# Kernel tuning notes

Hardware: AMD Instinct MI355X
Metric: run time of the kernel (lower is better)

Reference implementation:

```python
import jax, jax.numpy as jnp
import numpy as np

COLUMNS = 1024
CELLS = 16
NUM_CELLS = COLUMNS * CELLS
SEGS = 32
SYNS = 128
PERM_THR = 0.5
ACT_THR = 10
VOL_LR = 0.1


def _predictive(conn, vol, cons, active):
    # conn: [N,S,Y] int, vol/cons: [N,S,Y] float, active: [N] bool -> [N] bool
    connected = (vol > PERM_THR) | (cons > PERM_THR)
    pre = active[jnp.clip(conn, 0, NUM_CELLS - 1)]
    cnt = jnp.sum(connected & pre, axis=-1)          # active synapses per segment
    return jnp.any(cnt >= ACT_THR, axis=-1)         # cell predictive if any segment fires


def setup_inputs() -> dict:
    key = jax.random.key(0)
    k1, k2, k3, k4, k5 = jax.random.split(key, 5)
    x = jax.random.randint(k1, (COLUMNS,), 0, 2, dtype=jnp.int32)
    prev_active_cells = jax.random.bernoulli(k2, 0.5, (NUM_CELLS,))
    distal_connections = jax.random.randint(k3, (NUM_CELLS, SEGS, SYNS), 0, NUM_CELLS, dtype=jnp.int32)
    volatile_permanences = jax.random.uniform(k4, (NUM_CELLS, SEGS, SYNS), dtype=jnp.float32)
    consolidated_permanences = jax.random.uniform(k5, (NUM_CELLS, SEGS, SYNS), dtype=jnp.float32)
    return {
        'x': x,
        'modulation_signal': jnp.float32(1.0),
        'prev_active_cells': prev_active_cells,
        'distal_connections': distal_connections,
        'volatile_permanences': volatile_permanences,
        'consolidated_permanences': consolidated_permanences,
    }


def reference(x, modulation_signal, prev_active_cells, distal_connections,
              volatile_permanences, consolidated_permanences):
    col_active = x > 0                                              # [C]
    pred1 = _predictive(distal_connections, volatile_permanences,
                        consolidated_permanences, prev_active_cells).reshape(COLUMNS, CELLS)
    col_has_pred = jnp.any(pred1, axis=-1)                          # [C]
    cell_mask = jnp.where(col_has_pred[:, None], pred1, True)       # burst if no prediction
    new_active = (cell_mask & col_active[:, None]).reshape(-1)      # [N] bool (= winner cells)
    n_act = jnp.sum(col_active)
    n_pred = jnp.sum(col_active & col_has_pred)
    acc = jnp.where(n_act > 0,
                    n_pred.astype(jnp.float32) / jnp.maximum(n_act, 1).astype(jnp.float32),
                    jnp.float32(1.0))
    # Phase 2: learn on best-matching segment of each winner cell (volatile permanences)
    pre_prev = prev_active_cells[jnp.clip(distal_connections, 0, NUM_CELLS - 1)]  # [N,S,Y]
    overlaps = jnp.sum(pre_prev, axis=-1)                           # [N,S]
    best_seg = jnp.argmax(overlaps, axis=-1)                        # [N]
    seg_sel = best_seg[:, None] == jnp.arange(SEGS)[None, :]        # [N,S] bool
    learn_on = (modulation_signal != 0.0) & jnp.any(prev_active_cells)
    upd = new_active[:, None, None] & seg_sel[:, :, None] & learn_on  # [N,S,Y]
    delta = modulation_signal * VOL_LR * jnp.where(pre_prev, 1.0, -1.0)
    vol2 = jnp.clip(volatile_permanences + jnp.where(upd, delta, 0.0), 0.0, 1.0)
    # Phase 3: predictive state for next step, computed from new active cells
    pred2 = _predictive(distal_connections, vol2,
                        consolidated_permanences, new_active).reshape(COLUMNS, CELLS)
    new_predictive = (pred2 & col_active[:, None]).reshape(-1)
    return new_active, new_predictive, acc
```

## Files before the change

kernel.cpp:

```cpp
#include <hip/hip_runtime.h>
#include <stdint.h>

#define COLUMNS   1024
#define CELLS     16
#define NUM_CELLS (COLUMNS * CELLS)
#define SEGS      32
#define SYNS      128
#define ACT_THR   10
#define NB        2048
#define NWAVES    (NB * 4)

typedef int            i32x4 __attribute__((ext_vector_type(4)));
typedef float          f32x4 __attribute__((ext_vector_type(4)));

template<typename T>
__device__ __forceinline__ T ntload(const T* p) { return __builtin_nontemporal_load(p); }

__global__ __launch_bounds__(256) void pack_kernel(
    const void* __restrict__ prev, uint32_t* __restrict__ prevbits)
{
    __shared__ int s_isu8;
    const int t = threadIdx.x;
    if (t == 0) s_isu8 = 0;
    __syncthreads();
    const int* pi = (const int*)prev;
    int bad = 0;
    for (int k = t; k < NUM_CELLS / 4; k += 256)
        bad |= ((unsigned)pi[k] > 1u) ? 1 : 0;
    unsigned long long bb = __ballot(bad != 0);
    if ((t & 63) == 0 && bb) atomicOr(&s_isu8, 1);
    __syncthreads();

    if (t < 32) {
        const int w = blockIdx.x * 32 + t;
        uint32_t m = 0;
        if (s_isu8) {
            const unsigned char* p = (const unsigned char*)prev + (size_t)w * 32;
            #pragma unroll
            for (int j = 0; j < 32; ++j) m |= (p[j] ? 1u : 0u) << j;
        } else {
            const int* p = pi + (size_t)w * 32;
            #pragma unroll
            for (int j = 0; j < 32; ++j) m |= (p[j] ? 1u : 0u) << j;
        }
        prevbits[w] = m;
    }
}

__global__ __launch_bounds__(256) void p1_kernel(
    const uint32_t* __restrict__ prevbits, const int* __restrict__ x,
    const int* __restrict__ conn, const float* __restrict__ vol,
    const float* __restrict__ cons,
    unsigned char* __restrict__ pred1, unsigned char* __restrict__ bestseg)
{
    __shared__ uint32_t sbits[NUM_CELLS / 32];
    __shared__ unsigned short sacols[COLUMNS];
    __shared__ int s_gcnt[16], s_goff[16], s_acount;
    const int t = threadIdx.x, wv = t >> 6, ln = t & 63;

    for (int i = t; i < NUM_CELLS / 32; i += 256) sbits[i] = prevbits[i];

    int ca_[4];
    #pragma unroll
    for (int c2 = 0; c2 < 4; ++c2) {
        const int col = c2 * 256 + t;
        ca_[c2] = (x[col] != 0) ? 1 : 0;
        unsigned long long b = __ballot(ca_[c2] != 0);
        if (ln == 0) s_gcnt[c2 * 4 + wv] = __popcll(b);
    }
    __syncthreads();
    if (t == 0) {
        int s = 0;
        #pragma unroll
        for (int g = 0; g < 16; ++g) { s_goff[g] = s; s += s_gcnt[g]; }
        s_acount = s;
    }
    __syncthreads();
    #pragma unroll
    for (int c2 = 0; c2 < 4; ++c2) {
        unsigned long long b = __ballot(ca_[c2] != 0);
        if (ca_[c2])
            sacols[s_goff[c2 * 4 + wv] + __popcll(b & ((1ULL << ln) - 1ULL))] =
                (unsigned short)(c2 * 256 + t);
    }
    __syncthreads();

    const int nc   = s_acount * CELLS;
    const int half = ln >> 5;
    const int l32  = ln & 31;
    const int gw   = blockIdx.x * 4 + wv;

    for (int idx = gw; idx < nc; idx += NWAVES) {
        const int cell = (int)sacols[idx >> 4] * CELLS + (idx & 15);
        const size_t base = (size_t)cell * (SEGS * SYNS);
        int fire = 0, bestkey = 0;
        #pragma unroll 4
        for (int k = 0; k < 16; ++k) {
            const int segA = k * 2;
            const size_t off = base + (size_t)(segA + half) * SYNS + l32 * 4;
            i32x4 c = ntload((const i32x4*)(conn + off));
            int i0 = min(max(c.x, 0), NUM_CELLS - 1);
            int i1 = min(max(c.y, 0), NUM_CELLS - 1);
            int i2 = min(max(c.z, 0), NUM_CELLS - 1);
            int i3 = min(max(c.w, 0), NUM_CELLS - 1);
            int p0 = (sbits[i0 >> 5] >> (i0 & 31)) & 1;
            int p1 = (sbits[i1 >> 5] >> (i1 & 31)) & 1;
            int p2 = (sbits[i2 >> 5] >> (i2 & 31)) & 1;
            int p3 = (sbits[i3 >> 5] >> (i3 & 31)) & 1;
            unsigned long long bp0 = __ballot(p0 != 0);
            unsigned long long bp1 = __ballot(p1 != 0);
            unsigned long long bp2 = __ballot(p2 != 0);
            unsigned long long bp3 = __ballot(p3 != 0);
            int oA = __popcll(bp0 & 0xFFFFFFFFull) + __popcll(bp1 & 0xFFFFFFFFull)
                   + __popcll(bp2 & 0xFFFFFFFFull) + __popcll(bp3 & 0xFFFFFFFFull);
            int oB = __popcll(bp0 >> 32) + __popcll(bp1 >> 32)
                   + __popcll(bp2 >> 32) + __popcll(bp3 >> 32);
            bestkey = max(bestkey, (oA << 8) | (255 - segA));
            bestkey = max(bestkey, (oB << 8) | (254 - segA));
            if (!fire) {
                f32x4 v = ntload((const f32x4*)(vol + off));
                f32x4 q = ntload((const f32x4*)(cons + off));
                int cn0 = ((v.x > 0.5f) || (q.x > 0.5f)) ? 1 : 0;
                int cn1 = ((v.y > 0.5f) || (q.y > 0.5f)) ? 1 : 0;
                int cn2 = ((v.z > 0.5f) || (q.z > 0.5f)) ? 1 : 0;
                int cn3 = ((v.w > 0.5f) || (q.w > 0.5f)) ? 1 : 0;
                unsigned long long bc0 = __ballot(cn0 && p0);
                unsigned long long bc1 = __ballot(cn1 && p1);
                unsigned long long bc2 = __ballot(cn2 && p2);
                unsigned long long bc3 = __ballot(cn3 && p3);
                int cA = __popcll(bc0 & 0xFFFFFFFFull) + __popcll(bc1 & 0xFFFFFFFFull)
                       + __popcll(bc2 & 0xFFFFFFFFull) + __popcll(bc3 & 0xFFFFFFFFull);
                int cB = __popcll(bc0 >> 32) + __popcll(bc1 >> 32)
                       + __popcll(bc2 >> 32) + __popcll(bc3 >> 32);
                fire |= (cA >= ACT_THR) | (cB >= ACT_THR);
            }
        }
        if (ln == 0) {
            pred1[cell]   = (unsigned char)(fire ? 1 : 0);
            bestseg[cell] = (unsigned char)(255 - (bestkey & 0xFF));
        }
    }
}

__global__ __launch_bounds__(256) void p3_kernel(
    const uint32_t* __restrict__ prevbits, const int* __restrict__ x,
    const float* __restrict__ mod, const int* __restrict__ conn,
    const float* __restrict__ vol, const float* __restrict__ cons,
    const unsigned char* __restrict__ pred1, const unsigned char* __restrict__ bestseg,
    float* __restrict__ out)
{
    __shared__ uint32_t sprev[NUM_CELLS / 32];
    __shared__ uint32_t snew[NUM_CELLS / 32];
    __shared__ unsigned short sacols[COLUMNS];
    __shared__ unsigned short s_na[COLUMNS];
    __shared__ unsigned char s_act[COLUMNS];
    __shared__ int s_any, s_gcnt[16], s_goff[16], s_acount, s_nact, s_npred;
    const int t = threadIdx.x, wv = t >> 6, ln = t & 63;
    if (t == 0) { s_any = 0; s_nact = 0; s_npred = 0; }
    __syncthreads();

    {
        int any = 0;
        for (int i = t; i < NUM_CELLS / 32; i += 256) {
            uint32_t m = prevbits[i];
            sprev[i] = m;
            any |= (m != 0) ? 1 : 0;
        }
        unsigned long long ba = __ballot(any != 0);
        if (ln == 0 && ba) atomicOr(&s_any, 1);
    }

    int ca_[4];
    #pragma unroll
    for (int c2 = 0; c2 < 4; ++c2) {
        const int col = c2 * 256 + t;
        const int ca = (x[col] != 0) ? 1 : 0;
        ca_[c2] = ca;
        s_act[col] = (unsigned char)ca;
        uint4 pv = *(const uint4*)(pred1 + (size_t)col * CELLS);
        const int hp = ((pv.x | pv.y | pv.z | pv.w) != 0) ? 1 : 0;
        unsigned int bits = 0;
        if (ca) {
            if (hp) {
                #pragma unroll
                for (int b = 0; b < 4; ++b) {
                    unsigned int w = (&pv.x)[b];
                    bits |= ((w & 0xFFu) ? 1u : 0u) << (b * 4 + 0);
                    bits |= ((w & 0xFF00u) ? 1u : 0u) << (b * 4 + 1);
                    bits |= ((w & 0xFF0000u) ? 1u : 0u) << (b * 4 + 2);
                    bits |= ((w & 0xFF000000u) ? 1u : 0u) << (b * 4 + 3);
                }
            } else bits = 0xFFFFu;
        }
        s_na[col] = (unsigned short)bits;
        unsigned long long b1 = __ballot(ca != 0);
        unsigned long long b2 = __ballot((ca && hp) != 0);
        if (ln == 0) {
            s_gcnt[c2 * 4 + wv] = __popcll(b1);
            if (blockIdx.x == 0) {
                atomicAdd(&s_nact, __popcll(b1));
                atomicAdd(&s_npred, __popcll(b2));
            }
        }
    }
    __syncthreads();
    for (int w = t; w < NUM_CELLS / 32; w += 256)
        snew[w] = (uint32_t)s_na[2 * w] | ((uint32_t)s_na[2 * w + 1] << 16);
    if (t == 0) {
        int s = 0;
        #pragma unroll
        for (int g = 0; g < 16; ++g) { s_goff[g] = s; s += s_gcnt[g]; }
        s_acount = s;
    }
    __syncthreads();
    #pragma unroll
    for (int c2 = 0; c2 < 4; ++c2) {
        unsigned long long b = __ballot(ca_[c2] != 0);
        if (ca_[c2])
            sacols[s_goff[c2 * 4 + wv] + __popcll(b & ((1ULL << ln) - 1ULL))] =
                (unsigned short)(c2 * 256 + t);
    }

    float* outpred = out + NUM_CELLS;
    {
        const int i = blockIdx.x * 256 + t;
        if (i < NUM_CELLS && !s_act[i >> 4]) outpred[i] = 0.0f;
    }
    if (blockIdx.x == 0) {
        for (int g = t; g < NUM_CELLS / 4; g += 256) {
            const uint32_t w = snew[g >> 3];
            const int sh = (g & 7) * 4;
            f32x4 o;
            o.x = (w >> (sh + 0)) & 1 ? 1.0f : 0.0f;
            o.y = (w >> (sh + 1)) & 1 ? 1.0f : 0.0f;
            o.z = (w >> (sh + 2)) & 1 ? 1.0f : 0.0f;
            o.w = (w >> (sh + 3)) & 1 ? 1.0f : 0.0f;
            *(f32x4*)(out + (size_t)g * 4) = o;
        }
    }
    __syncthreads();
    if (blockIdx.x == 0 && t == 0)
        out[2 * NUM_CELLS] = (s_nact > 0)
            ? (float)s_npred / (float)max(s_nact, 1) : 1.0f;

    const int nc   = s_acount * CELLS;
    const int lf   = ((mod[0] != 0.0f) && s_any) ? 1 : 0;
    const float d  = mod[0] * 0.1f;
    const int half = ln >> 5;
    const int l32  = ln & 31;
    const int gw   = blockIdx.x * 4 + wv;

    for (int idx = gw; idx < nc; idx += NWAVES) {
        const int cell = (int)sacols[idx >> 4] * CELLS + (idx & 15);
        const size_t base = (size_t)cell * (SEGS * SYNS);
        const int na  = (snew[cell >> 5] >> (cell & 31)) & 1;
        const int upd = (lf && na) ? (int)bestseg[cell] : -1;
        int fire = 0;
        for (int k = 0; k < 16; ++k) {
            const int seg = k * 2 + half;
            const size_t off = base + (size_t)seg * SYNS + l32 * 4;
            i32x4 c = ntload((const i32x4*)(conn + off));
            f32x4 v = ntload((const f32x4*)(vol + off));
            f32x4 q = ntload((const f32x4*)(cons + off));
            int i0 = min(max(c.x, 0), NUM_CELLS - 1);
            int i1 = min(max(c.y, 0), NUM_CELLS - 1);
            int i2 = min(max(c.z, 0), NUM_CELLS - 1);
            int i3 = min(max(c.w, 0), NUM_CELLS - 1);
            float vx = v.x, vy = v.y, vz = v.z, vw = v.w;
            if (seg == upd) {
                int pp0 = (sprev[i0 >> 5] >> (i0 & 31)) & 1;
                int pp1 = (sprev[i1 >> 5] >> (i1 & 31)) & 1;
                int pp2 = (sprev[i2 >> 5] >> (i2 & 31)) & 1;
                int pp3 = (sprev[i3 >> 5] >> (i3 & 31)) & 1;
                vx += pp0 ? d : -d; vy += pp1 ? d : -d;
                vz += pp2 ? d : -d; vw += pp3 ? d : -d;
            }
            int cn0 = (vx > 0.5f) || (q.x > 0.5f);
            int cn1 = (vy > 0.5f) || (q.y > 0.5f);
            int cn2 = (vz > 0.5f) || (q.z > 0.5f);
            int cn3 = (vw > 0.5f) || (q.w > 0.5f);
            int pn0 = (snew[i0 >> 5] >> (i0 & 31)) & 1;
            int pn1 = (snew[i1 >> 5] >> (i1 & 31)) & 1;
            int pn2 = (snew[i2 >> 5] >> (i2 & 31)) & 1;
            int pn3 = (snew[i3 >> 5] >> (i3 & 31)) & 1;
            unsigned long long b0 = __ballot(cn0 && pn0);
            unsigned long long b1 = __ballot(cn1 && pn1);
            unsigned long long b2 = __ballot(cn2 && pn2);
            unsigned long long b3 = __ballot(cn3 && pn3);
            int cA = __popcll(b0 & 0xFFFFFFFFull) + __popcll(b1 & 0xFFFFFFFFull)
                   + __popcll(b2 & 0xFFFFFFFFull) + __popcll(b3 & 0xFFFFFFFFull);
            int cB = __popcll(b0 >> 32) + __popcll(b1 >> 32)
                   + __popcll(b2 >> 32) + __popcll(b3 >> 32);
            fire |= (cA >= ACT_THR) | (cB >= ACT_THR);
            if (fire) break;
        }
        if (ln == 0) outpred[cell] = fire ? 1.0f : 0.0f;
    }
}

extern "C" void kernel_launch(void* const* d_in, const int* in_sizes, int n_in,
                              void* d_out, int out_size, void* d_ws, size_t ws_size,
                              hipStream_t stream) {
    const int*   x    = (const int*)d_in[0];
    const float* mod  = (const float*)d_in[1];
    const void*  prev = d_in[2];
    const int*   conn = (const int*)d_in[3];
    const float* vol  = (const float*)d_in[4];
    const float* cons = (const float*)d_in[5];
    float* out = (float*)d_out;

    char* ws = (char*)d_ws;
    uint32_t* prevbits       = (uint32_t*)(ws + 0);
    unsigned char* pred1     = (unsigned char*)(ws + 16384);
    unsigned char* bestseg   = (unsigned char*)(ws + 32768);

    pack_kernel<<<16, 256, 0, stream>>>(prev, prevbits);
    p1_kernel<<<NB, 256, 0, stream>>>(prevbits, x, conn, vol, cons, pred1, bestseg);
    p3_kernel<<<NB, 256, 0, stream>>>(prevbits, x, mod, conn, vol, cons, pred1,
                                      bestseg, out);
}
```

Before: 51.60 us.

## Peel first segment in p1, skip vol/cons loads once fired, pack predictions as bits

The p1 kernel now evaluates segment pair 0 up front, including the connected check. If that pair already fires, the remaining segments only load connections for the best-segment overlap and skip the volatile and consolidated permanence reads. Phase-1 predictions become a bitmask built with atomicOr and cleared in pack_kernel, which makes the per-column check in p3 simpler. Nontemporal loads are replaced with ordinary loads in both kernels, which changes caching between p1 and p3, and the atomics add some contention.

```diff
diff --git a/kernel.cpp b/kernel.cpp
--- a/kernel.cpp
+++ b/kernel.cpp
@@ -13,11 +13,9 @@
 typedef int            i32x4 __attribute__((ext_vector_type(4)));
 typedef float          f32x4 __attribute__((ext_vector_type(4)));
 
-template<typename T>
-__device__ __forceinline__ T ntload(const T* p) { return __builtin_nontemporal_load(p); }
-
 __global__ __launch_bounds__(256) void pack_kernel(
-    const void* __restrict__ prev, uint32_t* __restrict__ prevbits)
+    const void* __restrict__ prev, uint32_t* __restrict__ prevbits,
+    uint32_t* __restrict__ predw)
 {
     __shared__ int s_isu8;
     const int t = threadIdx.x;
@@ -44,6 +42,7 @@
             for (int j = 0; j < 32; ++j) m |= (p[j] ? 1u : 0u) << j;
         }
         prevbits[w] = m;
+        predw[w] = 0;
     }
 }
 
@@ -51,7 +50,7 @@
     const uint32_t* __restrict__ prevbits, const int* __restrict__ x,
     const int* __restrict__ conn, const float* __restrict__ vol,
     const float* __restrict__ cons,
-    unsigned char* __restrict__ pred1, unsigned char* __restrict__ bestseg)
+    uint32_t* __restrict__ predw, unsigned char* __restrict__ bestseg)
 {
     __shared__ uint32_t sbits[NUM_CELLS / 32];
     __shared__ unsigned short sacols[COLUMNS];
@@ -94,11 +93,12 @@
         const int cell = (int)sacols[idx >> 4] * CELLS + (idx & 15);
         const size_t base = (size_t)cell * (SEGS * SYNS);
         int fire = 0, bestkey = 0;
-        #pragma unroll 4
-        for (int k = 0; k < 16; ++k) {
-            const int segA = k * 2;
-            const size_t off = base + (size_t)(segA + half) * SYNS + l32 * 4;
-            i32x4 c = ntload((const i32x4*)(conn + off));
+
+        {
+            const size_t off = base + (size_t)half * SYNS + l32 * 4;
+            i32x4 c = *(const i32x4*)(conn + off);
+            f32x4 v = *(const f32x4*)(vol + off);
+            f32x4 q = *(const f32x4*)(cons + off);
             int i0 = min(max(c.x, 0), NUM_CELLS - 1);
             int i1 = min(max(c.y, 0), NUM_CELLS - 1);
             int i2 = min(max(c.z, 0), NUM_CELLS - 1);
@@ -107,46 +107,111 @@
             int p1 = (sbits[i1 >> 5] >> (i1 & 31)) & 1;
             int p2 = (sbits[i2 >> 5] >> (i2 & 31)) & 1;
             int p3 = (sbits[i3 >> 5] >> (i3 & 31)) & 1;
+            int cn0 = ((v.x > 0.5f) || (q.x > 0.5f)) ? 1 : 0;
+            int cn1 = ((v.y > 0.5f) || (q.y > 0.5f)) ? 1 : 0;
+            int cn2 = ((v.z > 0.5f) || (q.z > 0.5f)) ? 1 : 0;
+            int cn3 = ((v.w > 0.5f) || (q.w > 0.5f)) ? 1 : 0;
+            unsigned long long bc0 = __ballot(cn0 && p0);
+            unsigned long long bc1 = __ballot(cn1 && p1);
+            unsigned long long bc2 = __ballot(cn2 && p2);
+            unsigned long long bc3 = __ballot(cn3 && p3);
             unsigned long long bp0 = __ballot(p0 != 0);
             unsigned long long bp1 = __ballot(p1 != 0);
             unsigned long long bp2 = __ballot(p2 != 0);
             unsigned long long bp3 = __ballot(p3 != 0);
+            int cA = __popcll(bc0 & 0xFFFFFFFFull) + __popcll(bc1 & 0xFFFFFFFFull)
+                   + __popcll(bc2 & 0xFFFFFFFFull) + __popcll(bc3 & 0xFFFFFFFFull);
+            int cB = __popcll(bc0 >> 32) + __popcll(bc1 >> 32)
+                   + __popcll(bc2 >> 32) + __popcll(bc3 >> 32);
             int oA = __popcll(bp0 & 0xFFFFFFFFull) + __popcll(bp1 & 0xFFFFFFFFull)
                    + __popcll(bp2 & 0xFFFFFFFFull) + __popcll(bp3 & 0xFFFFFFFFull);
             int oB = __popcll(bp0 >> 32) + __popcll(bp1 >> 32)
                    + __popcll(bp2 >> 32) + __popcll(bp3 >> 32);
-            bestkey = max(bestkey, (oA << 8) | (255 - segA));
-            bestkey = max(bestkey, (oB << 8) | (254 - segA));
-            if (!fire) {
-                f32x4 v = ntload((const f32x4*)(vol + off));
-                f32x4 q = ntload((const f32x4*)(cons + off));
-                int cn0 = ((v.x > 0.5f) || (q.x > 0.5f)) ? 1 : 0;
-                int cn1 = ((v.y > 0.5f) || (q.y > 0.5f)) ? 1 : 0;
-                int cn2 = ((v.z > 0.5f) || (q.z > 0.5f)) ? 1 : 0;
-                int cn3 = ((v.w > 0.5f) || (q.w > 0.5f)) ? 1 : 0;
-                unsigned long long bc0 = __ballot(cn0 && p0);
-                unsigned long long bc1 = __ballot(cn1 && p1);
-                unsigned long long bc2 = __ballot(cn2 && p2);
-                unsigned long long bc3 = __ballot(cn3 && p3);
-                int cA = __popcll(bc0 & 0xFFFFFFFFull) + __popcll(bc1 & 0xFFFFFFFFull)
-                       + __popcll(bc2 & 0xFFFFFFFFull) + __popcll(bc3 & 0xFFFFFFFFull);
-                int cB = __popcll(bc0 >> 32) + __popcll(bc1 >> 32)
-                       + __popcll(bc2 >> 32) + __popcll(bc3 >> 32);
-                fire |= (cA >= ACT_THR) | (cB >= ACT_THR);
+            fire = (cA >= ACT_THR) | (cB >= ACT_THR);
+            bestkey = max((oA << 8) | 255, (oB << 8) | 254);
+        }
+
+        if (fire) {
+            #pragma unroll
+            for (int k = 1; k < 16; ++k) {
+                const int segA = k * 2;
+                const size_t off = base + (size_t)(segA + half) * SYNS + l32 * 4;
+                i32x4 c = *(const i32x4*)(conn + off);
+                int i0 = min(max(c.x, 0), NUM_CELLS - 1);
+                int i1 = min(max(c.y, 0), NUM_CELLS - 1);
+                int i2 = min(max(c.z, 0), NUM_CELLS - 1);
+                int i3 = min(max(c.w, 0), NUM_CELLS - 1);
+                int p0 = (sbits[i0 >> 5] >> (i0 & 31)) & 1;
+                int p1 = (sbits[i1 >> 5] >> (i1 & 31)) & 1;
+                int p2 = (sbits[i2 >> 5] >> (i2 & 31)) & 1;
+                int p3 = (sbits[i3 >> 5] >> (i3 & 31)) & 1;
+                unsigned long long bp0 = __ballot(p0 != 0);
+                unsigned long long bp1 = __ballot(p1 != 0);
+                unsigned long long bp2 = __ballot(p2 != 0);
+                unsigned long long bp3 = __ballot(p3 != 0);
+                int oA = __popcll(bp0 & 0xFFFFFFFFull) + __popcll(bp1 & 0xFFFFFFFFull)
+                       + __popcll(bp2 & 0xFFFFFFFFull) + __popcll(bp3 & 0xFFFFFFFFull);
+                int oB = __popcll(bp0 >> 32) + __popcll(bp1 >> 32)
+                       + __popcll(bp2 >> 32) + __popcll(bp3 >> 32);
+                bestkey = max(bestkey, (oA << 8) | (255 - segA));
+                bestkey = max(bestkey, (oB << 8) | (254 - segA));
             }
-        }
+        } else {
+            #pragma unroll 4
+            for (int k = 1; k < 16; ++k) {
+                const int segA = k * 2;
+                const size_t off = base + (size_t)(segA + half) * SYNS + l32 * 4;
+                i32x4 c = *(const i32x4*)(conn + off);
+                int i0 = min(max(c.x, 0), NUM_CELLS - 1);
+                int i1 = min(max(c.y, 0), NUM_CELLS - 1);
+                int i2 = min(max(c.z, 0), NUM_CELLS - 1);
+                int i3 = min(max(c.w, 0), NUM_CELLS - 1);
+                int p0 = (sbits[i0 >> 5] >> (i0 & 31)) & 1;
+                int p1 = (sbits[i1 >> 5] >> (i1 & 31)) & 1;
+                int p2 = (sbits[i2 >> 5] >> (i2 & 31)) & 1;
+                int p3 = (sbits[i3 >> 5] >> (i3 & 31)) & 1;
+                unsigned long long bp0 = __ballot(p0 != 0);
+                unsigned long long bp1 = __ballot(p1 != 0);
+                unsigned long long bp2 = __ballot(p2 != 0);
+                unsigned long long bp3 = __ballot(p3 != 0);
+                int oA = __popcll(bp0 & 0xFFFFFFFFull) + __popcll(bp1 & 0xFFFFFFFFull)
+                       + __popcll(bp2 & 0xFFFFFFFFull) + __popcll(bp3 & 0xFFFFFFFFull);
+                int oB = __popcll(bp0 >> 32) + __popcll(bp1 >> 32)
+                       + __popcll(bp2 >> 32) + __popcll(bp3 >> 32);
+                bestkey = max(bestkey, (oA << 8) | (255 - segA));
+                bestkey = max(bestkey, (oB << 8) | (254 - segA));
+                if (!fire) {
+                    f32x4 v = *(const f32x4*)(vol + off);
+                    f32x4 q = *(const f32x4*)(cons + off);
+                    int cn0 = ((v.x > 0.5f) || (q.x > 0.5f)) ? 1 : 0;
+                    int cn1 = ((v.y > 0.5f) || (q.y > 0.5f)) ? 1 : 0;
+                    int cn2 = ((v.z > 0.5f) || (q.z > 0.5f)) ? 1 : 0;
+                    int cn3 = ((v.w > 0.5f) || (q.w > 0.5f)) ? 1 : 0;
+                    unsigned long long bc0 = __ballot(cn0 && p0);
+                    unsigned long long bc1 = __ballot(cn1 && p1);
+                    unsigned long long bc2 = __ballot(cn2 && p2);
+                    unsigned long long bc3 = __ballot(cn3 && p3);
+                    int cA = __popcll(bc0 & 0xFFFFFFFFull) + __popcll(bc1 & 0xFFFFFFFFull)
+                           + __popcll(bc2 & 0xFFFFFFFFull) + __popcll(bc3 & 0xFFFFFFFFull);
+                    int cB = __popcll(bc0 >> 32) + __popcll(bc1 >> 32)
+                           + __popcll(bc2 >> 32) + __popcll(bc3 >> 32);
+                    fire |= (cA >= ACT_THR) | (cB >= ACT_THR);
+                }
+            }
+        }
+
         if (ln == 0) {
-            pred1[cell]   = (unsigned char)(fire ? 1 : 0);
+            if (fire) atomicOr(&predw[cell >> 5], 1u << (cell & 31));
             bestseg[cell] = (unsigned char)(255 - (bestkey & 0xFF));
         }
     }
 }
 
 __global__ __launch_bounds__(256) void p3_kernel(
-    const uint32_t* __restrict__ prevbits, const int* __restrict__ x,
-    const float* __restrict__ mod, const int* __restrict__ conn,
-    const float* __restrict__ vol, const float* __restrict__ cons,
-    const unsigned char* __restrict__ pred1, const unsigned char* __restrict__ bestseg,
+    const uint32_t* __restrict__ prevbits, const uint32_t* __restrict__ predw,
+    const int* __restrict__ x, const float* __restrict__ mod,
+    const int* __restrict__ conn, const float* __restrict__ vol,
+    const float* __restrict__ cons, const unsigned char* __restrict__ bestseg,
     float* __restrict__ out)
 {
     __shared__ uint32_t sprev[NUM_CELLS / 32];
@@ -177,21 +242,11 @@
         const int ca = (x[col] != 0) ? 1 : 0;
         ca_[c2] = ca;
         s_act[col] = (unsigned char)ca;
-        uint4 pv = *(const uint4*)(pred1 + (size_t)col * CELLS);
-        const int hp = ((pv.x | pv.y | pv.z | pv.w) != 0) ? 1 : 0;
+        const uint32_t w = predw[col >> 1];
+        const unsigned int pb = (col & 1) ? (w >> 16) : (w & 0xFFFFu);
+        const int hp = (pb != 0) ? 1 : 0;
         unsigned int bits = 0;
-        if (ca) {
-            if (hp) {
-                #pragma unroll
-                for (int b = 0; b < 4; ++b) {
-                    unsigned int w = (&pv.x)[b];
-                    bits |= ((w & 0xFFu) ? 1u : 0u) << (b * 4 + 0);
-                    bits |= ((w & 0xFF00u) ? 1u : 0u) << (b * 4 + 1);
-                    bits |= ((w & 0xFF0000u) ? 1u : 0u) << (b * 4 + 2);
-                    bits |= ((w & 0xFF000000u) ? 1u : 0u) << (b * 4 + 3);
-                }
-            } else bits = 0xFFFFu;
-        }
+        if (ca) bits = hp ? pb : 0xFFFFu;
         s_na[col] = (unsigned short)bits;
         unsigned long long b1 = __ballot(ca != 0);
         unsigned long long b2 = __ballot((ca && hp) != 0);
@@ -259,9 +314,9 @@
         for (int k = 0; k < 16; ++k) {
             const int seg = k * 2 + half;
             const size_t off = base + (size_t)seg * SYNS + l32 * 4;
-            i32x4 c = ntload((const i32x4*)(conn + off));
-            f32x4 v = ntload((const f32x4*)(vol + off));
-            f32x4 q = ntload((const f32x4*)(cons + off));
+            i32x4 c = *(const i32x4*)(conn + off);
+            f32x4 v = *(const f32x4*)(vol + off);
+            f32x4 q = *(const f32x4*)(cons + off);
             int i0 = min(max(c.x, 0), NUM_CELLS - 1);
             int i1 = min(max(c.y, 0), NUM_CELLS - 1);
             int i2 = min(max(c.z, 0), NUM_CELLS - 1);
@@ -310,12 +365,12 @@
     float* out = (float*)d_out;
 
     char* ws = (char*)d_ws;
-    uint32_t* prevbits       = (uint32_t*)(ws + 0);
-    unsigned char* pred1     = (unsigned char*)(ws + 16384);
-    unsigned char* bestseg   = (unsigned char*)(ws + 32768);
-
-    pack_kernel<<<16, 256, 0, stream>>>(prev, prevbits);
-    p1_kernel<<<NB, 256, 0, stream>>>(prevbits, x, conn, vol, cons, pred1, bestseg);
-    p3_kernel<<<NB, 256, 0, stream>>>(prevbits, x, mod, conn, vol, cons, pred1,
+    uint32_t* prevbits     = (uint32_t*)(ws + 0);
+    uint32_t* predw        = (uint32_t*)(ws + 4096);
+    unsigned char* bestseg = (unsigned char*)(ws + 32768);
+
+    pack_kernel<<<16, 256, 0, stream>>>(prev, prevbits, predw);
+    p1_kernel<<<NB, 256, 0, stream>>>(prevbits, x, conn, vol, cons, predw, bestseg);
+    p3_kernel<<<NB, 256, 0, stream>>>(prevbits, predw, x, mod, conn, vol, cons,
                                       bestseg, out);
 }
```

Result: faster. 45.95 us (median of 2 runs) (-10.9%).
